# Kernel tuning notes

Hardware: AMD Instinct MI355X
Metric: run time of the kernel (lower is better)

Reference implementation:

```python
import jax, jax.numpy as jnp
import numpy as np

N = 16384
H = 2048
E = 8
I_PER_E = 8192 // E  # expert_intermediate_size = 1024


def setup_inputs() -> dict:
    key = jax.random.key(0)
    k1, k2, k3, k4 = jax.random.split(key, 4)
    hidden_states = jax.random.normal(k1, (N, H), dtype=jnp.float32)
    # sort_idx is a permutation of [0, N): tokens sorted by expert assignment
    sort_idx = jax.random.permutation(k2, N).astype(jnp.int64)
    # kaiming_uniform_ with a=sqrt(5): bound = sqrt(6/((1+a^2)*fan_in)) = 1/sqrt(fan_in)
    bound = 1.0 / np.sqrt(H)
    gate_up_proj = jax.random.uniform(k3, (E, H, 2 * I_PER_E), dtype=jnp.float32,
                                      minval=-bound, maxval=bound)
    # original inits down_proj to zeros; use small random so backward is non-trivial
    down_proj = jax.random.normal(k4, (E, I_PER_E, H), dtype=jnp.float32) * 0.02
    return {"hidden_states": hidden_states, "sort_idx": sort_idx,
            "gate_up_proj": gate_up_proj, "down_proj": down_proj}


def reference(hidden_states, sort_idx, gate_up_proj, down_proj):
    n, h = hidden_states.shape
    e = gate_up_proj.shape[0]
    chunk = n // e
    # gather tokens into expert order: [E, chunk, H]
    sorted_x = hidden_states[sort_idx].reshape(e, chunk, h)
    # fused gate+up grouped GEMM: [E, chunk, 2*I/E]
    gu = jnp.einsum('ech,ehf->ecf', sorted_x, gate_up_proj)
    gate, up = jnp.split(gu, 2, axis=-1)
    activated = jax.nn.silu(gate) * up  # [E, chunk, I/E]
    sorted_out = jnp.einsum('eci,eih->ech', activated, down_proj).reshape(n, h)
    # scatter back: out[sort_idx] = sorted_out
    out = jnp.zeros((n, h), dtype=sorted_out.dtype).at[sort_idx].set(sorted_out)
    return out
```

## Files before the change

### kernel.cpp

```cpp
#include <hip/hip_runtime.h>
#include <hip/hip_bf16.h>

#define N_TOK 16384
#define H_DIM 2048
#define NE 8
#define CHUNK 2048
#define IPE 1024
#define F2 2048

typedef __bf16 bf16;
typedef bf16 bf16x8 __attribute__((ext_vector_type(8)));
typedef float f32x4 __attribute__((ext_vector_type(4)));

typedef __attribute__((address_space(1))) void gvoid;
typedef __attribute__((address_space(3))) void svoid;

__device__ __forceinline__ void gload_lds16(const void* g, void* l) {
  __builtin_amdgcn_global_load_lds((gvoid*)g, (svoid*)l, 16, 0, 0);
}
__device__ __forceinline__ f32x4 MF(bf16x8 a, bf16x8 b, f32x4 c) {
  return __builtin_amdgcn_mfma_f32_16x16x32_bf16(a, b, c, 0, 0, 0);
}

#define BAR() __builtin_amdgcn_s_barrier()
#define LGKM0() asm volatile("s_waitcnt lgkmcnt(0)" ::: "memory")
#define LGKM8() asm volatile("s_waitcnt lgkmcnt(8)" ::: "memory")
#define VM6() asm volatile("s_waitcnt vmcnt(6)" ::: "memory")
#define VM0() asm volatile("s_waitcnt vmcnt(0)" ::: "memory")
#define PRIO(x) __builtin_amdgcn_s_setprio(x)
#define SCHED0() __builtin_amdgcn_sched_barrier(0)

__global__ __launch_bounds__(256) void k_prep(
    const float* __restrict__ hidden, const int* __restrict__ sidx,
    const float* __restrict__ w1, const float* __restrict__ w2,
    bf16* __restrict__ xs, bf16* __restrict__ w1t, bf16* __restrict__ w2t) {
  int b = blockIdx.x;
  int tid = threadIdx.x;
  if (b < 16384) {
    int row = b;
    int src = sidx[row];
    const float4* ip = (const float4*)(hidden + (size_t)src * H_DIM);
    float4 f0 = ip[tid * 2], f1 = ip[tid * 2 + 1];
    bf16x8 v;
    v[0] = (bf16)f0.x; v[1] = (bf16)f0.y; v[2] = (bf16)f0.z; v[3] = (bf16)f0.w;
    v[4] = (bf16)f1.x; v[5] = (bf16)f1.y; v[6] = (bf16)f1.z; v[7] = (bf16)f1.w;
    *(bf16x8*)(xs + (size_t)row * H_DIM + tid * 8) = v;
    return;
  }
  __shared__ bf16 lds[64][68];
  if (b < 24576) {
    int i1 = b - 16384;
    int fB = i1 & 31, hB = (i1 >> 5) & 31, e = i1 >> 10;
    const float* ip = w1 + ((size_t)e * H_DIM + hB * 64) * F2;
#pragma unroll
    for (int p = 0; p < 4; ++p) {
      int idx = p * 256 + tid;
      int half = idx >> 9, rem = idx & 511;
      int row = rem >> 3, c4 = rem & 7;
      float4 v = *(const float4*)(ip + (size_t)row * F2 + half * 1024 + fB * 32 + c4 * 4);
      bf16* d = &lds[row][half * 32 + c4 * 4];
      d[0] = (bf16)v.x; d[1] = (bf16)v.y; d[2] = (bf16)v.z; d[3] = (bf16)v.w;
    }
    __syncthreads();
    int fl = tid >> 2, hseg = (tid & 3) * 16;
    int g = fl >> 4, w = fl & 15;
    int lcol = ((g >> 1) << 4) + w + ((g & 1) << 5);
    bf16 v[16];
#pragma unroll
    for (int j = 0; j < 16; ++j) v[j] = lds[hseg + j][lcol];
    bf16* op = w1t + ((size_t)e * F2 + fB * 64 + fl) * H_DIM + hB * 64 + hseg;
    *(bf16x8*)op = *(bf16x8*)&v[0];
    *(bf16x8*)(op + 8) = *(bf16x8*)&v[8];
  } else {
    int i2 = b - 24576;
    int hB = i2 & 31, iB = (i2 >> 5) & 15, e = i2 >> 9;
    const float* ip = w2 + (size_t)e * IPE * H_DIM + (size_t)iB * 64 * H_DIM + hB * 64;
#pragma unroll
    for (int p = 0; p < 4; ++p) {
      int idx = p * 256 + tid;
      int row = idx >> 4, c4 = idx & 15;
      float4 v = *(const float4*)(ip + (size_t)row * H_DIM + c4 * 4);
      bf16* d = &lds[row][c4 * 4];
      d[0] = (bf16)v.x; d[1] = (bf16)v.y; d[2] = (bf16)v.z; d[3] = (bf16)v.w;
    }
    __syncthreads();
    int hl = tid >> 2, iseg = (tid & 3) * 16;
    bf16 v[16];
#pragma unroll
    for (int j = 0; j < 16; ++j) v[j] = lds[iseg + j][hl];
    bf16* op = w2t + ((size_t)e * H_DIM + hB * 64 + hl) * IPE + iB * 64 + iseg;
    *(bf16x8*)op = *(bf16x8*)&v[0];
    *(bf16x8*)(op + 8) = *(bf16x8*)&v[8];
  }
}

template <int KDIM, bool SILU>
__global__ __launch_bounds__(512, 2) void k_gemm8(
    const bf16* __restrict__ Aptr, const bf16* __restrict__ Bptr,
    const int* __restrict__ sidx, bf16* __restrict__ act,
    float* __restrict__ fout) {
  extern __shared__ char smem[];
  const int tid = threadIdx.x, lane = tid & 63, wv = tid >> 6;
  const int wm = wv >> 2, wn = wv & 3;
  constexpr int NT = KDIM / 64;

  int swzwg = (blockIdx.x & 7) * (gridDim.x >> 3) + (blockIdx.x >> 3);
  const int e = swzwg >> 6, bm = (swzwg >> 3) & 7, bn = swzwg & 7;

  const char* Ab = (const char*)(Aptr + ((size_t)e * CHUNK + bm * 256) * KDIM);
  const char* Bb = (const char*)(Bptr + ((size_t)e * 2048 + bn * 256) * KDIM);

  const int L0 = wv * 1024 + lane * 16;
  const int lin0 = L0 ^ (((L0 >> 7) & 7) << 4);
  const int srow0 = lin0 >> 7, scolb = lin0 & 127;

  const int rA = lane & 15;
  const int swzr = (rA & 7) << 4;
  const int cb = (lane >> 4) * 16;

  const char* pA0 = smem + wm * 16384 + rA * 128 + ((0 * 64 + cb) ^ swzr);
  const char* pA1 = smem + wm * 16384 + rA * 128 + ((1 * 64 + cb) ^ swzr);
  const char* pB0 = smem + 32768 + (wn >> 1) * 16384 + (wn & 1) * 8192 +
                    rA * 128 + ((0 * 64 + cb) ^ swzr);
  const char* pB1 = smem + 32768 + (wn >> 1) * 16384 + (wn & 1) * 8192 +
                    rA * 128 + ((1 * 64 + cb) ^ swzr);

  f32x4 acc[8][4] = {};

  auto stage = [&](int buf, int mat, int half, int kt) {
    const char* gb = (mat == 0) ? Ab : Bb;
    char* ld = smem + buf * 65536 + mat * 32768 + half * 16384 + wv * 1024;
    size_t rb = (size_t)(half * 128 + srow0) * (KDIM * 2) + (size_t)kt * 128 + scolb;
    gload_lds16(gb + rb, ld);
    gload_lds16(gb + rb + (size_t)64 * (KDIM * 2), ld + 8192);
  };

  stage(0, 1, 0, 0); stage(0, 1, 1, 0); stage(0, 0, 0, 0); stage(0, 0, 1, 0);
  stage(1, 1, 0, 1); stage(1, 1, 1, 1); stage(1, 0, 0, 1);
  VM6();
  BAR();

  auto ktile = [&](int t, int cur) {
    const int nxt = cur ^ 1;
    const int bo = cur * 65536;
    const char* a0 = pA0 + bo;
    const char* a1 = pA1 + bo;
    const char* b0p = pB0 + bo;
    const char* b1p = pB1 + bo;
    bf16x8 AA[4][2], B0[2][2], B1[2][2];
#pragma unroll
    for (int mi = 0; mi < 4; ++mi) {
      AA[mi][0] = *(const bf16x8*)(a0 + mi * 2048);
      AA[mi][1] = *(const bf16x8*)(a1 + mi * 2048);
    }
#pragma unroll
    for (int ni = 0; ni < 2; ++ni) {
      B0[ni][0] = *(const bf16x8*)(b0p + ni * 2048);
      B0[ni][1] = *(const bf16x8*)(b1p + ni * 2048);
    }
    if (t + 1 < NT) stage(nxt, 0, 1, t + 1);
    LGKM8();
    BAR();
    LGKM0();
    SCHED0();
    PRIO(1);
#pragma unroll
    for (int mi = 0; mi < 4; ++mi)
#pragma unroll
      for (int ni = 0; ni < 2; ++ni) {
        acc[mi][ni] = MF(AA[mi][0], B0[ni][0], acc[mi][ni]);
        acc[mi][ni] = MF(AA[mi][1], B0[ni][1], acc[mi][ni]);
      }
    PRIO(0);
    BAR();
#pragma unroll
    for (int ni = 0; ni < 2; ++ni) {
      B1[ni][0] = *(const bf16x8*)(b0p + (2 + ni) * 2048);
      B1[ni][1] = *(const bf16x8*)(b1p + (2 + ni) * 2048);
    }
    if (t + 2 < NT) stage(cur, 1, 0, t + 2);
    BAR();
    LGKM0();
    SCHED0();
    PRIO(1);
#pragma unroll
    for (int mi = 0; mi < 4; ++mi)
#pragma unroll
      for (int ni = 0; ni < 2; ++ni) {
        acc[mi][2 + ni] = MF(AA[mi][0], B1[ni][0], acc[mi][2 + ni]);
        acc[mi][2 + ni] = MF(AA[mi][1], B1[ni][1], acc[mi][2 + ni]);
      }
    PRIO(0);
    BAR();
#pragma unroll
    for (int mi = 0; mi < 4; ++mi) {
      AA[mi][0] = *(const bf16x8*)(a0 + (4 + mi) * 2048);
      AA[mi][1] = *(const bf16x8*)(a1 + (4 + mi) * 2048);
    }
    if (t + 2 < NT) stage(cur, 1, 1, t + 2);
    BAR();
    LGKM0();
    SCHED0();
    PRIO(1);
#pragma unroll
    for (int mi = 0; mi < 4; ++mi)
#pragma unroll
      for (int ni = 0; ni < 2; ++ni) {
        acc[4 + mi][ni] = MF(AA[mi][0], B0[ni][0], acc[4 + mi][ni]);
        acc[4 + mi][ni] = MF(AA[mi][1], B0[ni][1], acc[4 + mi][ni]);
      }
    PRIO(0);
    BAR();
    if (t + 2 < NT) {
      stage(cur, 0, 0, t + 2);
      VM6();
    } else if (t + 1 < NT) {
      VM0();
    }
    BAR();
    PRIO(1);
#pragma unroll
    for (int mi = 0; mi < 4; ++mi)
#pragma unroll
      for (int ni = 0; ni < 2; ++ni) {
        acc[4 + mi][2 + ni] = MF(AA[mi][0], B1[ni][0], acc[4 + mi][2 + ni]);
        acc[4 + mi][2 + ni] = MF(AA[mi][1], B1[ni][1], acc[4 + mi][2 + ni]);
      }
    PRIO(0);
    BAR();
  };

  for (int tt = 0; tt < NT; tt += 2) {
    ktile(tt, 0);
    ktile(tt + 1, 1);
  }

  if constexpr (SILU) {
    bf16* actp = act + ((size_t)e * CHUNK + bm * 256 + wm * 128) * IPE;
    const int r0 = (lane >> 4) * 4;
    const int c0 = bn * 128 + wn * 32 + (lane & 15);
#pragma unroll
    for (int mi = 0; mi < 8; ++mi)
#pragma unroll
      for (int p = 0; p < 2; ++p) {
        f32x4 g = acc[mi][2 * p], u = acc[mi][2 * p + 1];
#pragma unroll
        for (int r = 0; r < 4; ++r) {
          float gv = g[r];
          float a = gv / (1.f + __expf(-gv)) * u[r];
          actp[(size_t)(mi * 16 + r0 + r) * IPE + c0 + p * 16] = (bf16)a;
        }
      }
  } else {
    const int* sp = sidx + e * CHUNK + bm * 256 + wm * 128;
    const int r0 = (lane >> 4) * 4;
    const int c0 = bn * 256 + wn * 64 + (lane & 15);
#pragma unroll
    for (int mi = 0; mi < 8; ++mi)
#pragma unroll
      for (int r = 0; r < 4; ++r) {
        int dst = sp[mi * 16 + r0 + r];
        float* op = fout + (size_t)dst * H_DIM + c0;
#pragma unroll
        for (int ni = 0; ni < 4; ++ni) op[ni * 16] = acc[mi][ni][r];
      }
  }
}

extern "C" void kernel_launch(void* const* d_in, const int* in_sizes, int n_in,
                              void* d_out, int out_size, void* d_ws, size_t ws_size,
                              hipStream_t stream) {
  const float* hidden = (const float*)d_in[0];
  const int* sidx = (const int*)d_in[1];
  const float* w1 = (const float*)d_in[2];
  const float* w2 = (const float*)d_in[3];
  float* out = (float*)d_out;

  char* ws = (char*)d_ws;
  bf16* xs  = (bf16*)(ws);
  bf16* w1t = (bf16*)(ws + (size_t)67108864);
  bf16* w2t = (bf16*)(ws + (size_t)134217728);
  bf16* act = (bf16*)(ws + (size_t)167772160);

  hipFuncSetAttribute((const void*)k_gemm8<H_DIM, true>,
                      hipFuncAttributeMaxDynamicSharedMemorySize, 131072);
  hipFuncSetAttribute((const void*)k_gemm8<IPE, false>,
                      hipFuncAttributeMaxDynamicSharedMemorySize, 131072);

  k_prep<<<dim3(28672), 256, 0, stream>>>(hidden, sidx, w1, w2, xs, w1t, w2t);
  k_gemm8<H_DIM, true><<<dim3(512), 512, 131072, stream>>>(xs, w1t, nullptr, act, nullptr);
  k_gemm8<IPE, false><<<dim3(512), 512, 131072, stream>>>(act, w2t, sidx, nullptr, out);
}
```

Before: 297.6 us.

## Move down_proj weight conversion into extra blocks of the first GEMM launch

The w2 fp32-to-bf16 transpose is removed from the prep kernel and done by 2048 extra blocks appended to the first grouped GEMM launch, each handling two 64x64 tiles. The idea is to let this memory-bound conversion run alongside or after the compute-bound GEMM blocks instead of lengthening the prep kernel. The GEMM block swizzle is hardcoded to 64 so that the larger grid does not change the tile mapping. A risk is that the extra blocks, each reserving 128KB of LDS, use up block slots and could delay the GEMM tail or add their own tail.

```diff
diff --git a/kernel.cpp b/kernel.cpp
--- a/kernel.cpp
+++ b/kernel.cpp
@@ -32,8 +32,8 @@
 
 __global__ __launch_bounds__(256) void k_prep(
     const float* __restrict__ hidden, const int* __restrict__ sidx,
-    const float* __restrict__ w1, const float* __restrict__ w2,
-    bf16* __restrict__ xs, bf16* __restrict__ w1t, bf16* __restrict__ w2t) {
+    const float* __restrict__ w1,
+    bf16* __restrict__ xs, bf16* __restrict__ w1t) {
   int b = blockIdx.x;
   int tid = threadIdx.x;
   if (b < 16384) {
@@ -48,63 +48,74 @@
     return;
   }
   __shared__ bf16 lds[64][68];
-  if (b < 24576) {
-    int i1 = b - 16384;
-    int fB = i1 & 31, hB = (i1 >> 5) & 31, e = i1 >> 10;
-    const float* ip = w1 + ((size_t)e * H_DIM + hB * 64) * F2;
-#pragma unroll
-    for (int p = 0; p < 4; ++p) {
-      int idx = p * 256 + tid;
-      int half = idx >> 9, rem = idx & 511;
-      int row = rem >> 3, c4 = rem & 7;
-      float4 v = *(const float4*)(ip + (size_t)row * F2 + half * 1024 + fB * 32 + c4 * 4);
-      bf16* d = &lds[row][half * 32 + c4 * 4];
-      d[0] = (bf16)v.x; d[1] = (bf16)v.y; d[2] = (bf16)v.z; d[3] = (bf16)v.w;
-    }
-    __syncthreads();
-    int fl = tid >> 2, hseg = (tid & 3) * 16;
-    int g = fl >> 4, w = fl & 15;
-    int lcol = ((g >> 1) << 4) + w + ((g & 1) << 5);
-    bf16 v[16];
-#pragma unroll
-    for (int j = 0; j < 16; ++j) v[j] = lds[hseg + j][lcol];
-    bf16* op = w1t + ((size_t)e * F2 + fB * 64 + fl) * H_DIM + hB * 64 + hseg;
-    *(bf16x8*)op = *(bf16x8*)&v[0];
-    *(bf16x8*)(op + 8) = *(bf16x8*)&v[8];
-  } else {
-    int i2 = b - 24576;
-    int hB = i2 & 31, iB = (i2 >> 5) & 15, e = i2 >> 9;
-    const float* ip = w2 + (size_t)e * IPE * H_DIM + (size_t)iB * 64 * H_DIM + hB * 64;
-#pragma unroll
-    for (int p = 0; p < 4; ++p) {
-      int idx = p * 256 + tid;
-      int row = idx >> 4, c4 = idx & 15;
-      float4 v = *(const float4*)(ip + (size_t)row * H_DIM + c4 * 4);
-      bf16* d = &lds[row][c4 * 4];
-      d[0] = (bf16)v.x; d[1] = (bf16)v.y; d[2] = (bf16)v.z; d[3] = (bf16)v.w;
-    }
-    __syncthreads();
-    int hl = tid >> 2, iseg = (tid & 3) * 16;
-    bf16 v[16];
-#pragma unroll
-    for (int j = 0; j < 16; ++j) v[j] = lds[iseg + j][hl];
-    bf16* op = w2t + ((size_t)e * H_DIM + hB * 64 + hl) * IPE + iB * 64 + iseg;
-    *(bf16x8*)op = *(bf16x8*)&v[0];
-    *(bf16x8*)(op + 8) = *(bf16x8*)&v[8];
-  }
+  int i1 = b - 16384;
+  int fB = i1 & 31, hB = (i1 >> 5) & 31, e = i1 >> 10;
+  const float* ip = w1 + ((size_t)e * H_DIM + hB * 64) * F2;
+#pragma unroll
+  for (int p = 0; p < 4; ++p) {
+    int idx = p * 256 + tid;
+    int half = idx >> 9, rem = idx & 511;
+    int row = rem >> 3, c4 = rem & 7;
+    float4 v = *(const float4*)(ip + (size_t)row * F2 + half * 1024 + fB * 32 + c4 * 4);
+    bf16* d = &lds[row][half * 32 + c4 * 4];
+    d[0] = (bf16)v.x; d[1] = (bf16)v.y; d[2] = (bf16)v.z; d[3] = (bf16)v.w;
+  }
+  __syncthreads();
+  int fl = tid >> 2, hseg = (tid & 3) * 16;
+  int g = fl >> 4, w = fl & 15;
+  int lcol = ((g >> 1) << 4) + w + ((g & 1) << 5);
+  bf16 v[16];
+#pragma unroll
+  for (int j = 0; j < 16; ++j) v[j] = lds[hseg + j][lcol];
+  bf16* op = w1t + ((size_t)e * F2 + fB * 64 + fl) * H_DIM + hB * 64 + hseg;
+  *(bf16x8*)op = *(bf16x8*)&v[0];
+  *(bf16x8*)(op + 8) = *(bf16x8*)&v[8];
 }
 
 template <int KDIM, bool SILU>
 __global__ __launch_bounds__(512, 2) void k_gemm8(
     const bf16* __restrict__ Aptr, const bf16* __restrict__ Bptr,
     const int* __restrict__ sidx, bf16* __restrict__ act,
-    float* __restrict__ fout) {
+    float* __restrict__ fout, const float* __restrict__ w2src,
+    bf16* __restrict__ w2t) {
   extern __shared__ char smem[];
-  const int tid = threadIdx.x, lane = tid & 63, wv = tid >> 6;
+  const int tid = threadIdx.x;
+
+  if constexpr (SILU) {
+    if (blockIdx.x >= 512) {
+      bf16(*lds)[68] = (bf16(*)[68])smem;
+#pragma unroll
+      for (int q = 0; q < 2; ++q) {
+        int tile = (blockIdx.x - 512) * 2 + q;
+        int hB = tile & 31, iB = (tile >> 5) & 15, e = tile >> 9;
+        const float* ip = w2src + (size_t)e * IPE * H_DIM +
+                          (size_t)iB * 64 * H_DIM + hB * 64;
+#pragma unroll
+        for (int p = 0; p < 2; ++p) {
+          int idx = p * 512 + tid;
+          int row = idx >> 4, c4 = idx & 15;
+          float4 v = *(const float4*)(ip + (size_t)row * H_DIM + c4 * 4);
+          bf16* d = &lds[row][c4 * 4];
+          d[0] = (bf16)v.x; d[1] = (bf16)v.y; d[2] = (bf16)v.z; d[3] = (bf16)v.w;
+        }
+        __syncthreads();
+        int hl = tid >> 3, iseg = (tid & 7) * 8;
+        bf16 v[8];
+#pragma unroll
+        for (int j = 0; j < 8; ++j) v[j] = lds[iseg + j][hl];
+        bf16* op = w2t + ((size_t)e * H_DIM + hB * 64 + hl) * IPE + iB * 64 + iseg;
+        *(bf16x8*)op = *(bf16x8*)&v[0];
+        __syncthreads();
+      }
+      return;
+    }
+  }
+
+  const int lane = tid & 63, wv = tid >> 6;
   const int wm = wv >> 2, wn = wv & 3;
   constexpr int NT = KDIM / 64;
 
-  int swzwg = (blockIdx.x & 7) * (gridDim.x >> 3) + (blockIdx.x >> 3);
+  int swzwg = (blockIdx.x & 7) * 64 + (blockIdx.x >> 3);
   const int e = swzwg >> 6, bm = (swzwg >> 3) & 7, bn = swzwg & 7;
 
   const char* Ab = (const char*)(Aptr + ((size_t)e * CHUNK + bm * 256) * KDIM);
@@ -118,12 +129,12 @@
   const int swzr = (rA & 7) << 4;
   const int cb = (lane >> 4) * 16;
 
-  const char* pA0 = smem + wm * 16384 + rA * 128 + ((0 * 64 + cb) ^ swzr);
-  const char* pA1 = smem + wm * 16384 + rA * 128 + ((1 * 64 + cb) ^ swzr);
+  const char* pA0 = smem + wm * 16384 + rA * 128 + ((0 + cb) ^ swzr);
+  const char* pA1 = smem + wm * 16384 + rA * 128 + ((64 + cb) ^ swzr);
   const char* pB0 = smem + 32768 + (wn >> 1) * 16384 + (wn & 1) * 8192 +
-                    rA * 128 + ((0 * 64 + cb) ^ swzr);
+                    rA * 128 + ((0 + cb) ^ swzr);
   const char* pB1 = smem + 32768 + (wn >> 1) * 16384 + (wn & 1) * 8192 +
-                    rA * 128 + ((1 * 64 + cb) ^ swzr);
+                    rA * 128 + ((64 + cb) ^ swzr);
 
   f32x4 acc[8][4] = {};
 
@@ -287,7 +298,9 @@
   hipFuncSetAttribute((const void*)k_gemm8<IPE, false>,
                       hipFuncAttributeMaxDynamicSharedMemorySize, 131072);
 
-  k_prep<<<dim3(28672), 256, 0, stream>>>(hidden, sidx, w1, w2, xs, w1t, w2t);
-  k_gemm8<H_DIM, true><<<dim3(512), 512, 131072, stream>>>(xs, w1t, nullptr, act, nullptr);
-  k_gemm8<IPE, false><<<dim3(512), 512, 131072, stream>>>(act, w2t, sidx, nullptr, out);
-}
+  k_prep<<<dim3(24576), 256, 0, stream>>>(hidden, sidx, w1, xs, w1t);
+  k_gemm8<H_DIM, true><<<dim3(2560), 512, 131072, stream>>>(
+      xs, w1t, nullptr, act, nullptr, w2, w2t);
+  k_gemm8<IPE, false><<<dim3(512), 512, 131072, stream>>>(
+      act, w2t, sidx, nullptr, out, nullptr, nullptr);
+}
```

After: 303.6 us. +2.0%, slower.
